# Kernel optimization log

Measured on AMD Instinct MI355X. Metric: run time of the kernel, lower is better.

The kernel has to match this reference:

```python
import jax, jax.numpy as jnp
import numpy as np

B, D, O, E, K = 8192, 2048, 2048, 8, 2


def setup_inputs() -> dict:
    key = jax.random.key(0)
    k1, k2, k3, k4 = jax.random.split(key, 4)
    x = jax.random.normal(k1, (B, D), dtype=jnp.float32)
    # router: Linear(D -> E)
    router_w = jax.random.normal(k2, (E, D), dtype=jnp.float32) * (1.0 / np.sqrt(D))
    router_b = jnp.zeros((E,), dtype=jnp.float32)
    # experts: [E, O, D] weight (xavier-uniform-like scale), [E, O] bias (zeros)
    lim = np.sqrt(6.0 / (D + O))
    expert_w = jax.random.uniform(k3, (E, O, D), dtype=jnp.float32, minval=-lim, maxval=lim)
    expert_b = jnp.zeros((E, O), dtype=jnp.float32)
    return {"x": x, "router_w": router_w, "router_b": router_b,
            "expert_w": expert_w, "expert_b": expert_b}


def reference(x, router_w, router_b, expert_w, expert_b):
    # router logits [B, E]
    logits = x @ router_w.T + router_b
    top_vals, top_idx = jax.lax.top_k(logits, K)          # [B, K]
    routing_weights = jax.nn.softmax(top_vals, axis=-1)   # softmax over top-k logits
    # dense per-(token, expert) combine weight [B, E]; zero for unselected experts
    onehot = jax.nn.one_hot(top_idx, E, dtype=x.dtype)    # [B, K, E]
    w_be = jnp.einsum('bk,bke->be', routing_weights, onehot)
    # per-expert linear, weighted combine (loop over small fixed E)
    out = jnp.zeros((x.shape[0], O), dtype=x.dtype)
    for e in range(E):
        out = out + w_be[:, e:e + 1] * (x @ expert_w[e].T + expert_b[e])
    return out
```

## Files before the change

### kernel.cpp

```cpp
#include <hip/hip_runtime.h>
#include <stdint.h>

#define NB 8192
#define ND 2048
#define NO 2048
#define NE 8
#define NT (ND / 32)

typedef __bf16 bf16x8 __attribute__((ext_vector_type(8)));
typedef float floatx4 __attribute__((ext_vector_type(4)));

__device__ __forceinline__ unsigned short f2bf(float f) {
    union { float f; uint32_t u; } v; v.f = f;
    uint32_t u = v.u;
    return (unsigned short)((u + 0x7FFFu + ((u >> 16) & 1u)) >> 16);
}

__global__ __launch_bounds__(256) void cvt_bf16_kernel(
        const float* __restrict__ b, unsigned short* __restrict__ ob, int n4) {
    int i = blockIdx.x * blockDim.x + threadIdx.x;
    int stride = gridDim.x * blockDim.x;
    for (; i < n4; i += stride) {
        float4 v = ((const float4*)b)[i];
        ushort4 o;
        o.x = f2bf(v.x); o.y = f2bf(v.y); o.z = f2bf(v.z); o.w = f2bf(v.w);
        ((ushort4*)ob)[i] = o;
    }
}

__global__ __launch_bounds__(256) void router_topk_kernel(const float* __restrict__ x,
        const float* __restrict__ rw, const float* __restrict__ rb,
        unsigned short* __restrict__ xbf,
        int* __restrict__ i0a, int* __restrict__ i1a,
        float* __restrict__ w0a, float* __restrict__ w1a) {
    const int wave = threadIdx.x >> 6;
    const int lane = threadIdx.x & 63;
    const int t = blockIdx.x * 4 + wave;
    const float4* xp = (const float4*)(x + (size_t)t * ND);
    const float4* rp = (const float4*)rw;
    ushort4* xo = (ushort4*)(xbf + (size_t)t * ND);
    float acc[NE];
#pragma unroll
    for (int e = 0; e < NE; e++) acc[e] = 0.f;
#pragma unroll
    for (int i = 0; i < ND / 256; i++) {
        int idx = i * 64 + lane;
        float4 xv = xp[idx];
        ushort4 o;
        o.x = f2bf(xv.x); o.y = f2bf(xv.y); o.z = f2bf(xv.z); o.w = f2bf(xv.w);
        xo[idx] = o;
#pragma unroll
        for (int e = 0; e < NE; e++) {
            float4 rv = rp[(size_t)e * (ND / 4) + idx];
            acc[e] += xv.x * rv.x + xv.y * rv.y + xv.z * rv.z + xv.w * rv.w;
        }
    }
#pragma unroll
    for (int e = 0; e < NE; e++) {
        float v = acc[e];
#pragma unroll
        for (int s = 32; s > 0; s >>= 1) v += __shfl_xor(v, s, 64);
        acc[e] = v;
    }
    if (lane == 0) {
        float lg[NE];
#pragma unroll
        for (int e = 0; e < NE; e++) lg[e] = acc[e] + rb[e];
        int i0 = 0; float v0 = lg[0];
#pragma unroll
        for (int e = 1; e < NE; e++) if (lg[e] > v0) { v0 = lg[e]; i0 = e; }
        int i1 = -1; float v1 = -3.4e38f;
#pragma unroll
        for (int e = 0; e < NE; e++) if (e != i0 && lg[e] > v1) { v1 = lg[e]; i1 = e; }
        float ex = expf(v1 - v0);
        float inv = 1.f / (1.f + ex);
        i0a[t] = i0; i1a[t] = i1;
        w0a[t] = inv; w1a[t] = ex * inv;
    }
}

__global__ __launch_bounds__(256) void compact_kernel(
        const int* __restrict__ i0a, const int* __restrict__ i1a,
        const float* __restrict__ w0a, const float* __restrict__ w1a,
        int* __restrict__ cnt, int* __restrict__ tok, float* __restrict__ wl) {
    const int lane = threadIdx.x & 63;
    const int gw = (blockIdx.x * 256 + threadIdx.x) >> 6;
    const int t = gw * 64 + lane;
#pragma unroll
    for (int which = 0; which < 2; which++) {
        int sel   = which ? i1a[t] : i0a[t];
        float w   = which ? w1a[t] : w0a[t];
        unsigned long long m[NE];
#pragma unroll
        for (int e = 0; e < NE; e++) m[e] = __ballot(sel == e);
        int slot = __popcll(m[sel] & ((1ull << lane) - 1ull));
        int base = 0;
        if (lane < NE) base = atomicAdd(&cnt[lane], (int)__popcll(m[lane]));
        base = __shfl(base, sel, 64);
        tok[sel * NB + base + slot] = t;
        wl[sel * NB + base + slot]  = w;
    }
}

#define GLL16(g, l) __builtin_amdgcn_global_load_lds( \
    (const __attribute__((address_space(1))) void*)(g), \
    (__attribute__((address_space(3))) void*)(l), 16, 0, 0)

__global__ __launch_bounds__(256, 3) void moe_gemm_kernel(
        const unsigned short* __restrict__ xbf, const unsigned short* __restrict__ wbf,
        const float* __restrict__ eb, const int* __restrict__ cntArr,
        const int* __restrict__ listTok, const float* __restrict__ listW,
        float* __restrict__ out) {
    __shared__ unsigned short sA[3][128 * 32];
    __shared__ unsigned short sB[3][128 * 32];
    __shared__ int sTok[128];
    __shared__ float sW[128];

    const int e = blockIdx.z, mt = blockIdx.y, nt = blockIdx.x;
    const int cnt = cntArr[e];
    if (mt * 128 >= cnt) return;
    const int tid = threadIdx.x;
    if (tid < 128) {
        int r = mt * 128 + tid;
        bool ok = r < cnt;
        sTok[tid] = ok ? listTok[e * NB + r] : 0;
        sW[tid]   = ok ? listW[e * NB + r] : 0.f;
    }
    __syncthreads();

    const char* gA[2]; const char* gB[2];
    int offAB[2];
#pragma unroll
    for (int r = 0; r < 2; r++) {
        int c = r * 256 + tid;
        int row = c >> 2, colb = (c & 3) * 16;
        gA[r] = (const char*)xbf + (size_t)sTok[row] * (ND * 2) + colb;
        gB[r] = (const char*)wbf + ((size_t)e * NO + (size_t)nt * 128 + row) * (ND * 2) + colb;
        offAB[r] = c * 16;
    }

    const int wave = tid >> 6, lane = tid & 63;
    const int wm = (wave >> 1) * 64, wn = (wave & 1) * 64;
    const int lr = lane & 15, lq = lane >> 4;
    int roA[4], roB[4];
#pragma unroll
    for (int i = 0; i < 4; i++) {
        roA[i] = (wm + i * 16 + lr) * 32 + lq * 8;
        roB[i] = (wn + i * 16 + lr) * 32 + lq * 8;
    }

    floatx4 acc[4][4];
#pragma unroll
    for (int mi = 0; mi < 4; mi++)
#pragma unroll
        for (int nj = 0; nj < 4; nj++) acc[mi][nj] = (floatx4){0.f, 0.f, 0.f, 0.f};

#pragma unroll
    for (int r = 0; r < 2; r++) {
        GLL16(gA[r], (char*)sA[0] + offAB[r]);
        GLL16(gB[r], (char*)sB[0] + offAB[r]);
        gA[r] += 64; gB[r] += 64;
    }
#pragma unroll
    for (int r = 0; r < 2; r++) {
        GLL16(gA[r], (char*)sA[1] + offAB[r]);
        GLL16(gB[r], (char*)sB[1] + offAB[r]);
        gA[r] += 64; gB[r] += 64;
    }

    int cur = 0;
#pragma unroll 1
    for (int t = 0; t < NT; t++) {
        int nxt = cur + 2; if (nxt >= 3) nxt -= 3;
        if (t + 2 < NT) {
#pragma unroll
            for (int r = 0; r < 2; r++) {
                GLL16(gA[r], (char*)sA[nxt] + offAB[r]);
                GLL16(gB[r], (char*)sB[nxt] + offAB[r]);
                gA[r] += 64; gB[r] += 64;
            }
            asm volatile("s_waitcnt vmcnt(8)" ::: "memory");
        } else if (t + 2 == NT) {
            asm volatile("s_waitcnt vmcnt(4)" ::: "memory");
        } else {
            asm volatile("s_waitcnt vmcnt(0)" ::: "memory");
        }
        __builtin_amdgcn_s_barrier();

        const unsigned short* sAc = sA[cur];
        const unsigned short* sBc = sB[cur];
        bf16x8 af[4], bfr[4];
#pragma unroll
        for (int mi = 0; mi < 4; mi++) af[mi] = *(const bf16x8*)&sAc[roA[mi]];
#pragma unroll
        for (int nj = 0; nj < 4; nj++) bfr[nj] = *(const bf16x8*)&sBc[roB[nj]];
#pragma unroll
        for (int mi = 0; mi < 4; mi++)
#pragma unroll
            for (int nj = 0; nj < 4; nj++)
                acc[mi][nj] = __builtin_amdgcn_mfma_f32_16x16x32_bf16(af[mi], bfr[nj], acc[mi][nj], 0, 0, 0);

        asm volatile("s_waitcnt lgkmcnt(0)" ::: "memory");
        __builtin_amdgcn_s_barrier();
        cur = cur + 1 == 3 ? 0 : cur + 1;
    }

#pragma unroll
    for (int nj = 0; nj < 4; nj++) {
        int gn = nt * 128 + wn + nj * 16 + lr;
        float bias = eb[(size_t)e * NO + gn];
#pragma unroll
        for (int mi = 0; mi < 4; mi++) {
#pragma unroll
            for (int r = 0; r < 4; r++) {
                int m = wm + mi * 16 + lq * 4 + r;
                if (mt * 128 + m < cnt) {
                    atomicAdd(out + (size_t)sTok[m] * NO + gn,
                              sW[m] * (acc[mi][nj][r] + bias));
                }
            }
        }
    }
}

extern "C" void kernel_launch(void* const* d_in, const int* in_sizes, int n_in,
                              void* d_out, int out_size, void* d_ws, size_t ws_size,
                              hipStream_t stream) {
    const float* x        = (const float*)d_in[0];
    const float* router_w = (const float*)d_in[1];
    const float* router_b = (const float*)d_in[2];
    const float* expert_w = (const float*)d_in[3];
    const float* expert_b = (const float*)d_in[4];
    float* out = (float*)d_out;
    char* ws = (char*)d_ws;

    unsigned short* xbf = (unsigned short*)ws;
    unsigned short* wbf = (unsigned short*)(ws + 33554432);
    size_t o = 100663296;
    int*   tokL = (int*)(ws + o);   o += NE * NB * 4;
    float* wL   = (float*)(ws + o); o += NE * NB * 4;
    int*   i0a  = (int*)(ws + o);   o += NB * 4;
    int*   i1a  = (int*)(ws + o);   o += NB * 4;
    float* w0a  = (float*)(ws + o); o += NB * 4;
    float* w1a  = (float*)(ws + o); o += NB * 4;
    int*   cnt  = (int*)(ws + o);   o += 128;

    hipMemsetAsync(cnt, 0, 128, stream);
    hipMemsetAsync(out, 0, (size_t)NB * NO * 4, stream);
    router_topk_kernel<<<NB / 4, 256, 0, stream>>>(x, router_w, router_b, xbf,
                                                   i0a, i1a, w0a, w1a);
    cvt_bf16_kernel<<<2048, 256, 0, stream>>>(expert_w, wbf, NE * NO * ND / 4);
    compact_kernel<<<NB / 64 / 4, 256, 0, stream>>>(i0a, i1a, w0a, w1a, cnt, tokL, wL);
    moe_gemm_kernel<<<dim3(NO / 128, NB / 128, NE), 256, 0, stream>>>(
        xbf, wbf, expert_b, cnt, tokL, wL, out);
}
```

Baseline: 591.4 us.

## Enlarge MoE GEMM tiles to 256x256x64 with swizzled LDS and fused zeroing

```diff
diff --git a/kernel.cpp b/kernel.cpp
--- a/kernel.cpp
+++ b/kernel.cpp
@@ -5,7 +5,10 @@
 #define ND 2048
 #define NO 2048
 #define NE 8
-#define NT (ND / 32)
+#define BK 64
+#define NT (ND / BK)
+#define BM 256
+#define BN 256
 
 typedef __bf16 bf16x8 __attribute__((ext_vector_type(8)));
 typedef float floatx4 __attribute__((ext_vector_type(4)));
@@ -16,15 +19,23 @@
     return (unsigned short)((u + 0x7FFFu + ((u >> 16) & 1u)) >> 16);
 }
 
-__global__ __launch_bounds__(256) void cvt_bf16_kernel(
-        const float* __restrict__ b, unsigned short* __restrict__ ob, int n4) {
+__global__ __launch_bounds__(256) void cvt_zero_kernel(
+        const float* __restrict__ w, unsigned short* __restrict__ ob,
+        float* __restrict__ out) {
+    const int n4W = NE * NO * ND / 4;
+    const int n4O = NB * NO / 4;
     int i = blockIdx.x * blockDim.x + threadIdx.x;
     int stride = gridDim.x * blockDim.x;
-    for (; i < n4; i += stride) {
-        float4 v = ((const float4*)b)[i];
-        ushort4 o;
-        o.x = f2bf(v.x); o.y = f2bf(v.y); o.z = f2bf(v.z); o.w = f2bf(v.w);
-        ((ushort4*)ob)[i] = o;
+    for (; i < n4W + n4O; i += stride) {
+        if (i < n4W) {
+            float4 v = ((const float4*)w)[i];
+            ushort4 o;
+            o.x = f2bf(v.x); o.y = f2bf(v.y); o.z = f2bf(v.z); o.w = f2bf(v.w);
+            ((ushort4*)ob)[i] = o;
+        } else {
+            float4 z = {0.f, 0.f, 0.f, 0.f};
+            ((float4*)out)[i - n4W] = z;
+        }
     }
 }
 
@@ -32,7 +43,9 @@
         const float* __restrict__ rw, const float* __restrict__ rb,
         unsigned short* __restrict__ xbf,
         int* __restrict__ i0a, int* __restrict__ i1a,
-        float* __restrict__ w0a, float* __restrict__ w1a) {
+        float* __restrict__ w0a, float* __restrict__ w1a,
+        int* __restrict__ cnt) {
+    if (blockIdx.x == 0 && threadIdx.x < NE) cnt[threadIdx.x] = 0;
     const int wave = threadIdx.x >> 6;
     const int lane = threadIdx.x & 63;
     const int t = blockIdx.x * 4 + wave;
@@ -106,118 +119,117 @@
     (const __attribute__((address_space(1))) void*)(g), \
     (__attribute__((address_space(3))) void*)(l), 16, 0, 0)
 
-__global__ __launch_bounds__(256, 3) void moe_gemm_kernel(
+__global__ __launch_bounds__(512, 2) void moe_gemm_kernel(
         const unsigned short* __restrict__ xbf, const unsigned short* __restrict__ wbf,
         const float* __restrict__ eb, const int* __restrict__ cntArr,
         const int* __restrict__ listTok, const float* __restrict__ listW,
         float* __restrict__ out) {
-    __shared__ unsigned short sA[3][128 * 32];
-    __shared__ unsigned short sB[3][128 * 32];
-    __shared__ int sTok[128];
-    __shared__ float sW[128];
+    __shared__ unsigned short sA[2][BM * BK];
+    __shared__ unsigned short sB[2][BN * BK];
 
     const int e = blockIdx.z, mt = blockIdx.y, nt = blockIdx.x;
     const int cnt = cntArr[e];
-    if (mt * 128 >= cnt) return;
+    if (mt * BM >= cnt) return;
     const int tid = threadIdx.x;
-    if (tid < 128) {
-        int r = mt * 128 + tid;
-        bool ok = r < cnt;
-        sTok[tid] = ok ? listTok[e * NB + r] : 0;
-        sW[tid]   = ok ? listW[e * NB + r] : 0.f;
-    }
-    __syncthreads();
-
-    const char* gA[2]; const char* gB[2];
-    int offAB[2];
-#pragma unroll
-    for (int r = 0; r < 2; r++) {
-        int c = r * 256 + tid;
-        int row = c >> 2, colb = (c & 3) * 16;
-        gA[r] = (const char*)xbf + (size_t)sTok[row] * (ND * 2) + colb;
-        gB[r] = (const char*)wbf + ((size_t)e * NO + (size_t)nt * 128 + row) * (ND * 2) + colb;
-        offAB[r] = c * 16;
+
+    const char* gA[4]; const char* gB[4];
+    int ldsOff[4];
+#pragma unroll
+    for (int i = 0; i < 4; i++) {
+        int cid = i * 512 + tid;
+        int prow = cid >> 3;
+        int pcol = (cid & 7) * 16;
+        int scol = pcol ^ ((prow & 7) << 4);
+        int gr = mt * BM + prow;
+        int tk = (gr < cnt) ? listTok[e * NB + gr] : 0;
+        gA[i] = (const char*)xbf + (size_t)tk * (ND * 2) + scol;
+        gB[i] = (const char*)wbf + ((size_t)e * NO + (size_t)nt * BN + prow) * (ND * 2) + scol;
+        ldsOff[i] = cid * 16;
     }
 
     const int wave = tid >> 6, lane = tid & 63;
-    const int wm = (wave >> 1) * 64, wn = (wave & 1) * 64;
+    const int wm = (wave >> 2) * 128;
+    const int wn = (wave & 3) * 64;
     const int lr = lane & 15, lq = lane >> 4;
-    int roA[4], roB[4];
-#pragma unroll
-    for (int i = 0; i < 4; i++) {
-        roA[i] = (wm + i * 16 + lr) * 32 + lq * 8;
-        roB[i] = (wn + i * 16 + lr) * 32 + lq * 8;
-    }
-
-    floatx4 acc[4][4];
-#pragma unroll
-    for (int mi = 0; mi < 4; mi++)
+    const int xorv = (lr & 7) << 4;
+    int roA[8], roB[4];
+#pragma unroll
+    for (int mi = 0; mi < 8; mi++) roA[mi] = (wm + mi * 16 + lr) * (BK * 2) + ((lq * 16) ^ xorv);
+#pragma unroll
+    for (int nj = 0; nj < 4; nj++) roB[nj] = (wn + nj * 16 + lr) * (BK * 2) + ((lq * 16) ^ xorv);
+
+    floatx4 acc[8][4];
+#pragma unroll
+    for (int mi = 0; mi < 8; mi++)
 #pragma unroll
         for (int nj = 0; nj < 4; nj++) acc[mi][nj] = (floatx4){0.f, 0.f, 0.f, 0.f};
 
 #pragma unroll
-    for (int r = 0; r < 2; r++) {
-        GLL16(gA[r], (char*)sA[0] + offAB[r]);
-        GLL16(gB[r], (char*)sB[0] + offAB[r]);
-        gA[r] += 64; gB[r] += 64;
-    }
-#pragma unroll
-    for (int r = 0; r < 2; r++) {
-        GLL16(gA[r], (char*)sA[1] + offAB[r]);
-        GLL16(gB[r], (char*)sB[1] + offAB[r]);
-        gA[r] += 64; gB[r] += 64;
-    }
-
-    int cur = 0;
+    for (int b = 0; b < 2; b++) {
+#pragma unroll
+        for (int i = 0; i < 4; i++) {
+            GLL16(gA[i], (char*)sA[b] + ldsOff[i]);
+            GLL16(gB[i], (char*)sB[b] + ldsOff[i]);
+            gA[i] += 2 * BK; gB[i] += 2 * BK;
+        }
+    }
+
 #pragma unroll 1
     for (int t = 0; t < NT; t++) {
-        int nxt = cur + 2; if (nxt >= 3) nxt -= 3;
-        if (t + 2 < NT) {
-#pragma unroll
-            for (int r = 0; r < 2; r++) {
-                GLL16(gA[r], (char*)sA[nxt] + offAB[r]);
-                GLL16(gB[r], (char*)sB[nxt] + offAB[r]);
-                gA[r] += 64; gB[r] += 64;
-            }
-            asm volatile("s_waitcnt vmcnt(8)" ::: "memory");
-        } else if (t + 2 == NT) {
-            asm volatile("s_waitcnt vmcnt(4)" ::: "memory");
-        } else {
-            asm volatile("s_waitcnt vmcnt(0)" ::: "memory");
-        }
+        const int cur = t & 1;
+        if (t + 1 < NT) { asm volatile("s_waitcnt vmcnt(8)" ::: "memory"); }
+        else           { asm volatile("s_waitcnt vmcnt(0)" ::: "memory"); }
         __builtin_amdgcn_s_barrier();
 
         const unsigned short* sAc = sA[cur];
         const unsigned short* sBc = sB[cur];
-        bf16x8 af[4], bfr[4];
-#pragma unroll
-        for (int mi = 0; mi < 4; mi++) af[mi] = *(const bf16x8*)&sAc[roA[mi]];
-#pragma unroll
-        for (int nj = 0; nj < 4; nj++) bfr[nj] = *(const bf16x8*)&sBc[roB[nj]];
-#pragma unroll
-        for (int mi = 0; mi < 4; mi++)
+#pragma unroll
+        for (int kk = 0; kk < 2; kk++) {
+            bf16x8 af[8], bfr[4];
+#pragma unroll
+            for (int mi = 0; mi < 8; mi++)
+                af[mi] = *(const bf16x8*)((const char*)sAc + (roA[mi] ^ (kk * 64)));
 #pragma unroll
             for (int nj = 0; nj < 4; nj++)
-                acc[mi][nj] = __builtin_amdgcn_mfma_f32_16x16x32_bf16(af[mi], bfr[nj], acc[mi][nj], 0, 0, 0);
+                bfr[nj] = *(const bf16x8*)((const char*)sBc + (roB[nj] ^ (kk * 64)));
+            __builtin_amdgcn_s_setprio(1);
+#pragma unroll
+            for (int mi = 0; mi < 8; mi++)
+#pragma unroll
+                for (int nj = 0; nj < 4; nj++)
+                    acc[mi][nj] = __builtin_amdgcn_mfma_f32_16x16x32_bf16(af[mi], bfr[nj], acc[mi][nj], 0, 0, 0);
+            __builtin_amdgcn_s_setprio(0);
+        }
 
         asm volatile("s_waitcnt lgkmcnt(0)" ::: "memory");
         __builtin_amdgcn_s_barrier();
-        cur = cur + 1 == 3 ? 0 : cur + 1;
-    }
-
-#pragma unroll
-    for (int nj = 0; nj < 4; nj++) {
-        int gn = nt * 128 + wn + nj * 16 + lr;
-        float bias = eb[(size_t)e * NO + gn];
-#pragma unroll
-        for (int mi = 0; mi < 4; mi++) {
-#pragma unroll
-            for (int r = 0; r < 4; r++) {
-                int m = wm + mi * 16 + lq * 4 + r;
-                if (mt * 128 + m < cnt) {
-                    atomicAdd(out + (size_t)sTok[m] * NO + gn,
-                              sW[m] * (acc[mi][nj][r] + bias));
-                }
+        if (t + 2 < NT) {
+#pragma unroll
+            for (int i = 0; i < 4; i++) {
+                GLL16(gA[i], (char*)sA[cur] + ldsOff[i]);
+                GLL16(gB[i], (char*)sB[cur] + ldsOff[i]);
+                gA[i] += 2 * BK; gB[i] += 2 * BK;
+            }
+        }
+    }
+
+    float bias[4];
+#pragma unroll
+    for (int nj = 0; nj < 4; nj++)
+        bias[nj] = eb[(size_t)e * NO + nt * BN + wn + nj * 16 + lr];
+#pragma unroll
+    for (int mi = 0; mi < 8; mi++) {
+#pragma unroll
+        for (int r = 0; r < 4; r++) {
+            int m = wm + mi * 16 + lq * 4 + r;
+            int gr = mt * BM + m;
+            if (gr < cnt) {
+                int tk   = listTok[e * NB + gr];
+                float wg = listW[e * NB + gr];
+                float* op = out + (size_t)tk * NO + nt * BN + wn + lr;
+#pragma unroll
+                for (int nj = 0; nj < 4; nj++)
+                    atomicAdd(op + nj * 16, wg * (acc[mi][nj][r] + bias[nj]));
             }
         }
     }
@@ -245,12 +257,10 @@
     float* w1a  = (float*)(ws + o); o += NB * 4;
     int*   cnt  = (int*)(ws + o);   o += 128;
 
-    hipMemsetAsync(cnt, 0, 128, stream);
-    hipMemsetAsync(out, 0, (size_t)NB * NO * 4, stream);
     router_topk_kernel<<<NB / 4, 256, 0, stream>>>(x, router_w, router_b, xbf,
-                                                   i0a, i1a, w0a, w1a);
-    cvt_bf16_kernel<<<2048, 256, 0, stream>>>(expert_w, wbf, NE * NO * ND / 4);
+                                                   i0a, i1a, w0a, w1a, cnt);
+    cvt_zero_kernel<<<2048, 256, 0, stream>>>(expert_w, wbf, out);
     compact_kernel<<<NB / 64 / 4, 256, 0, stream>>>(i0a, i1a, w0a, w1a, cnt, tokL, wL);
-    moe_gemm_kernel<<<dim3(NO / 128, NB / 128, NE), 256, 0, stream>>>(
+    moe_gemm_kernel<<<dim3(NO / BN, NB / BM, NE), 512, 0, stream>>>(
         xbf, wbf, expert_b, cnt, tokL, wL, out);
 }
```

After: 575.7 us. -2.7%, faster.
